# Performance work log

Measured on AMD Instinct MI355X. Metric: run time of the kernel, lower is better.

The kernel has to match this reference:

```python
import jax, jax.numpy as jnp
import numpy as np

B, S, H = 4, 1024, 2560          # batch, seq, hidden_size
E, K, F = 32, 6, 1536            # num_experts, top_k, moe_intermediate_size
SHARED_F = 2 * 1536              # moe_num_shared_experts * moe_intermediate_size
NORM_MIN = 1e-12                 # config.moe_norm_min


def setup_inputs() -> dict:
    key = jax.random.key(0)
    ks = jax.random.split(key, 9)
    rnd = lambda k, shape, scale=0.02: jax.random.normal(k, shape, dtype=jnp.float32) * scale
    return {
        "hidden_states": jax.random.normal(ks[0], (B, S, H), dtype=jnp.float32),
        "router_w": rnd(ks[1], (E, H)),              # Ernie4_5_MoeTopKRouter.weight (fp32)
        "router_bias": jnp.zeros((E,), jnp.float32),  # moe_statics.e_score_correction_bias
        "gate_w": rnd(ks[2], (E, H, F)),
        "up_w": rnd(ks[3], (E, H, F)),
        "down_w": rnd(ks[4], (E, F, H)),
        "shared_gate_w": rnd(ks[5], (H, SHARED_F)),
        "shared_up_w": rnd(ks[6], (H, SHARED_F)),
        "shared_down_w": rnd(ks[7], (SHARED_F, H)),
    }


def _mlp(x, gw, uw, dw):
    # Ernie4_5_MoeMLP: down( silu(gate(x)) * up(x) ), no biases
    return (jax.nn.silu(x @ gw) * (x @ uw)) @ dw


def _forward(hidden_states, router_w, router_bias, gate_w, up_w, down_w,
             shared_gate_w, shared_up_w, shared_down_w):
    T = B * S
    xt = hidden_states.reshape(T, H)

    # shared experts path (always-on dense MLP)
    shared_out = _mlp(xt, shared_gate_w, shared_up_w, shared_down_w)

    # router: fp32 linear -> softmax -> (+ correction bias) -> top-k -> renorm
    logits = xt.astype(jnp.float32) @ router_w.T            # [T, E]
    probs = jax.nn.softmax(logits, axis=-1)
    top_w, top_i = jax.lax.top_k(probs + router_bias[None, :], K)  # [T, K]
    top_w = top_w / jnp.clip(jnp.sum(top_w, axis=-1, keepdims=True), NORM_MIN)
    top_w = top_w.astype(hidden_states.dtype)

    # expert combine: loop over the fixed expert set; per-token combine weight
    # cw[t] = sum_k top_w[t,k] * (top_i[t,k] == e)  (matches one-hot dispatch +
    # index_add_ scatter combine of the original)
    out = jnp.zeros_like(xt)
    for e in range(E):
        cw = jnp.sum(jnp.where(top_i == e, top_w, 0.0), axis=-1)  # [T]
        y = _mlp(xt, gate_w[e], up_w[e], down_w[e])               # [T, H]
        out = out + cw[:, None] * y

    out = out + shared_out
    return out.reshape(B, S, H)


def reference(hidden_states, router_w, router_bias, gate_w, up_w, down_w,
              shared_gate_w, shared_up_w, shared_down_w):
    return _forward(hidden_states, router_w, router_bias, gate_w, up_w, down_w,
                    shared_gate_w, shared_up_w, shared_down_w)
```

## Files before the change

kernel.cpp:

```cpp
#include <hip/hip_runtime.h>
#include <hip/hip_bf16.h>
#include <math.h>

#define T_TOK 4096
#define HID   2560
#define NEXP  32
#define KTOP  6
#define FF    1536
#define SFF   3072
#define MAXP  (T_TOK*KTOP)

typedef __attribute__((ext_vector_type(8))) short short8;
typedef __attribute__((ext_vector_type(4))) float f32x4;

static __device__ __forceinline__ unsigned short f2bf(float x){
  return __builtin_bit_cast(unsigned short, (__bf16)x);
}

static __device__ __forceinline__ void gload_lds16(const void* g, void* l){
  __builtin_amdgcn_global_load_lds(
      (const __attribute__((address_space(1))) unsigned int*)g,
      (__attribute__((address_space(3))) unsigned int*)l, 16, 0, 0);
}

__global__ void k_cast_x(const float* __restrict__ x, unsigned short* __restrict__ xb){
  int i = (blockIdx.x * 256 + threadIdx.x) * 4;
  float4 v = *(const float4*)(x + i);
  ushort4 o;
  o.x = f2bf(v.x); o.y = f2bf(v.y); o.z = f2bf(v.z); o.w = f2bf(v.w);
  *(ushort4*)(xb + i) = o;
}

__global__ __launch_bounds__(256)
void k_transpose(const float* __restrict__ in, unsigned short* __restrict__ out,
                 const int R, const int C){
  const size_t bo = (size_t)blockIdx.z * (size_t)R * C;
  __shared__ unsigned short t2[64][72];
  const int r0 = blockIdx.y * 64, c0 = blockIdx.x * 64;
  const int tid = threadIdx.x;
  const int cr = tid & 15;
  const int rr = tid >> 4;
#pragma unroll
  for (int i = 0; i < 4; ++i){
    const int r = rr + 16*i;
    float4 v = *(const float4*)(in + bo + (size_t)(r0 + r)*C + c0 + cr*4);
    ushort4 p;
    p.x = f2bf(v.x); p.y = f2bf(v.y); p.z = f2bf(v.z); p.w = f2bf(v.w);
    *(ushort4*)(&t2[r][cr*4]) = p;
  }
  __syncthreads();
  const int rw = tid & 7;
  const int ro = tid >> 3;
#pragma unroll
  for (int i = 0; i < 2; ++i){
    const int c = ro + 32*i;
    ushort4 a, b;
    a.x = t2[rw*8+0][c]; a.y = t2[rw*8+1][c]; a.z = t2[rw*8+2][c]; a.w = t2[rw*8+3][c];
    b.x = t2[rw*8+4][c]; b.y = t2[rw*8+5][c]; b.z = t2[rw*8+6][c]; b.w = t2[rw*8+7][c];
    unsigned short* op = out + bo + (size_t)(c0 + c)*R + r0 + rw*8;
    *(ushort4*)(op)     = a;
    *(ushort4*)(op + 4) = b;
  }
}

__global__ void k_router(const float* __restrict__ x, const float* __restrict__ rw,
                         const float* __restrict__ rb, float* __restrict__ top_w,
                         int* __restrict__ top_i, int* __restrict__ counts){
  const int lane = threadIdx.x & 63;
  const int wv   = threadIdx.x >> 6;
  const int t    = blockIdx.x * 4 + wv;
  const float* xr = x + (size_t)t * HID;
  float xv[40];
#pragma unroll
  for (int i = 0; i < 40; ++i) xv[i] = xr[lane + 64*i];
  float sc[32];
  for (int e = 0; e < 32; ++e){
    const float* w = rw + (size_t)e * HID;
    float s = 0.f;
#pragma unroll
    for (int i = 0; i < 40; ++i) s = fmaf(xv[i], w[lane + 64*i], s);
#pragma unroll
    for (int o = 32; o; o >>= 1) s += __shfl_xor(s, o);
    sc[e] = s;
  }
  float mx = sc[0];
#pragma unroll
  for (int e = 1; e < 32; ++e) mx = fmaxf(mx, sc[e]);
  float se = 0.f;
#pragma unroll
  for (int e = 0; e < 32; ++e){ sc[e] = expf(sc[e] - mx); se += sc[e]; }
  const float inv = 1.f / se;
#pragma unroll
  for (int e = 0; e < 32; ++e) sc[e] = sc[e] * inv + rb[e];

  unsigned chosen = 0; float swv[KTOP]; int sid[KTOP]; float wsum = 0.f;
#pragma unroll
  for (int k = 0; k < KTOP; ++k){
    float bv = -1e30f; int bi = 0;
#pragma unroll
    for (int e = 0; e < 32; ++e){
      bool ok = !((chosen >> e) & 1u);
      if (ok && sc[e] > bv){ bv = sc[e]; bi = e; }
    }
    chosen |= 1u << bi; swv[k] = bv; sid[k] = bi; wsum += bv;
  }
  const float dn = fmaxf(wsum, 1e-12f);
  if (lane < KTOP){
    top_w[t*KTOP + lane] = swv[lane] / dn;
    top_i[t*KTOP + lane] = sid[lane];
    atomicAdd(counts + sid[lane], 1);
  }
}

__global__ void k_scan(const int* __restrict__ counts, int* __restrict__ offsets){
  if (threadIdx.x == 0){
    int a = 0;
    for (int e = 0; e < NEXP; ++e){ offsets[e] = a; a += counts[e]; }
    offsets[NEXP] = a;
  }
}

__global__ void k_scatter(const int* __restrict__ top_i, const float* __restrict__ top_w,
                          const int* __restrict__ offsets, int* __restrict__ cursor,
                          int* __restrict__ pair_tok, float* __restrict__ pair_w){
  const int t = blockIdx.x * 256 + threadIdx.x;
  if (t >= T_TOK) return;
#pragma unroll
  for (int k = 0; k < KTOP; ++k){
    int e = top_i[t*KTOP + k];
    int pos = offsets[e] + atomicAdd(cursor + e, 1);
    pair_tok[pos] = t;
    pair_w[pos]   = top_w[t*KTOP + k];
  }
}

template<bool EXP>
__global__ __launch_bounds__(256, 2)
void k_gateup3(const unsigned short* __restrict__ A,
               const unsigned short* __restrict__ BgT,
               const unsigned short* __restrict__ BuT,
               unsigned short* __restrict__ outp,
               const int* __restrict__ pair_tok,
               const int* __restrict__ counts, const int* __restrict__ offsets,
               const int N)
{
  constexpr int K = HID;
  constexpr int NT = K / 32;
  const int total = gridDim.x;
  const int phys  = blockIdx.x;
  const int logical = (phys & 7) * (total >> 3) + (phys >> 3);
  const int mt   = logical & 31;
  const int rest = logical >> 5;
  const int ntiles = N >> 7;
  const int n0 = (rest % ntiles) << 7;

  int M, base; const unsigned short *Bg, *Bu;
  if (EXP){
    const int e = rest / ntiles;
    M = counts[e]; base = offsets[e];
    const size_t wo = (size_t)e * (size_t)N * K;
    Bg = BgT + wo; Bu = BuT + wo;
  } else { M = T_TOK; base = 0; Bg = BgT; Bu = BuT; }
  if (mt * 128 >= M) return;

  __shared__ unsigned short As[3][4096];
  __shared__ unsigned short Bgs[3][4096];
  __shared__ unsigned short Bus[3][4096];

  const int tid  = threadIdx.x;
  const int lane = tid & 63;
  const int w    = tid >> 6;
  const int wr = w >> 1, wc = w & 1;

  const int lrow  = lane >> 2;
  const int chunk = lane & 3;
  const unsigned short *aptr[2], *bgptr[2], *buptr[2];
  int sw[2];
#pragma unroll
  for (int i = 0; i < 2; ++i){
    const int r = w*32 + i*16 + lrow;
    sw[i] = (chunk ^ (r & 3)) * 8;
    int ar = min(mt*128 + r, M - 1);
    int arow = EXP ? pair_tok[base + ar] : ar;
    aptr[i]  = A  + (size_t)arow * K;
    bgptr[i] = Bg + (size_t)(n0 + r) * K;
    buptr[i] = Bu + (size_t)(n0 + r) * K;
  }

  const f32x4 zero = {0.f,0.f,0.f,0.f};
  f32x4 accg[4][4], accu[4][4];
#pragma unroll
  for (int m = 0; m < 4; ++m)
#pragma unroll
    for (int n = 0; n < 4; ++n){ accg[m][n] = zero; accu[m][n] = zero; }

  const int am  = wr*64 + (lane & 15);
  const int bn_ = wc*64 + (lane & 15);
  const int fg  = ((lane >> 4) ^ (lane & 3)) * 16;

#define GU_STAGE(cb, k0)                                                   \
  {                                                                        \
    char* asd = (char*)As[cb]  + w*2048;                                   \
    char* bgd = (char*)Bgs[cb] + w*2048;                                   \
    char* bud = (char*)Bus[cb] + w*2048;                                   \
    _Pragma("unroll")                                                      \
    for (int i = 0; i < 2; ++i){                                           \
      gload_lds16(aptr[i]  + (k0) + sw[i], asd + i*1024);                  \
      gload_lds16(bgptr[i] + (k0) + sw[i], bgd + i*1024);                  \
      gload_lds16(buptr[i] + (k0) + sw[i], bud + i*1024);                  \
    }                                                                      \
  }

  GU_STAGE(0, 0)
  GU_STAGE(1, 32)
  asm volatile("s_waitcnt vmcnt(6)" ::: "memory");
  __builtin_amdgcn_s_barrier();

  int c0 = 0, c1 = 1, c2 = 2;
  for (int t = 0; t < NT; ++t){
    if (t + 2 < NT) GU_STAGE(c2, (t + 2) * 32)
    short8 af[4], bgf[4], buf_[4];
#pragma unroll
    for (int m = 0; m < 4; ++m)
      af[m] = *(const short8*)((const char*)As + c0*8192 + (am + m*16)*64 + fg);
#pragma unroll
    for (int n = 0; n < 4; ++n){
      bgf[n]  = *(const short8*)((const char*)Bgs + c0*8192 + (bn_ + n*16)*64 + fg);
      buf_[n] = *(const short8*)((const char*)Bus + c0*8192 + (bn_ + n*16)*64 + fg);
    }
#pragma unroll
    for (int m = 0; m < 4; ++m)
#pragma unroll
      for (int n = 0; n < 4; ++n){
        accg[m][n] = __builtin_amdgcn_mfma_f32_16x16x32_bf16(af[m], bgf[n],  accg[m][n], 0, 0, 0);
        accu[m][n] = __builtin_amdgcn_mfma_f32_16x16x32_bf16(af[m], buf_[n], accu[m][n], 0, 0, 0);
      }
    if (t + 2 < NT) asm volatile("s_waitcnt vmcnt(6)" ::: "memory");
    else            asm volatile("s_waitcnt vmcnt(0)" ::: "memory");
    __builtin_amdgcn_s_barrier();
    int tmp = c0; c0 = c1; c1 = c2; c2 = tmp;
  }
#undef GU_STAGE

#pragma unroll
  for (int m = 0; m < 4; ++m)
#pragma unroll
    for (int j = 0; j < 4; ++j){
      const int rr = mt*128 + wr*64 + m*16 + (lane >> 4)*4 + j;
      if (rr < M){
        unsigned short* orow = outp + (size_t)(base + rr) * N + n0 + wc*64 + (lane & 15);
#pragma unroll
        for (int n = 0; n < 4; ++n){
          float g = accg[m][n][j], u = accu[m][n][j];
          float s = (g / (1.f + expf(-g))) * u;
          orow[n*16] = f2bf(s);
        }
      }
    }
}

template<bool EXP>
__global__ __launch_bounds__(256, 3)
void k_down3(const unsigned short* __restrict__ Aact, const int K,
             const unsigned short* __restrict__ BT, float* __restrict__ outp,
             const int* __restrict__ pair_tok, const float* __restrict__ pair_w,
             const int* __restrict__ counts, const int* __restrict__ offsets)
{
  constexpr int N = HID;
  constexpr int ntiles = N >> 7;
  const int total = gridDim.x;
  const int phys  = blockIdx.x;
  const int logical = (phys & 7) * (total >> 3) + (phys >> 3);
  const int mt   = logical & 31;
  const int rest = logical >> 5;
  const int n0 = (rest % ntiles) << 7;

  int M, base; const unsigned short* Bw;
  if (EXP){
    const int e = rest / ntiles;
    M = counts[e]; base = offsets[e];
    Bw = BT + (size_t)e * (size_t)N * K;
  } else { M = T_TOK; base = 0; Bw = BT; }
  if (mt * 128 >= M) return;

  __shared__ unsigned short As[3][4096];
  __shared__ unsigned short Bs[3][4096];

  const int tid  = threadIdx.x;
  const int lane = tid & 63;
  const int w    = tid >> 6;
  const int wr = w >> 1, wc = w & 1;

  const int lrow  = lane >> 2;
  const int chunk = lane & 3;
  const unsigned short *aptr[2], *bptr[2];
  int sw[2];
#pragma unroll
  for (int i = 0; i < 2; ++i){
    const int r = w*32 + i*16 + lrow;
    sw[i] = (chunk ^ (r & 3)) * 8;
    int ar = min(mt*128 + r, M - 1);
    aptr[i] = Aact + (size_t)(base + ar) * K;
    bptr[i] = Bw + (size_t)(n0 + r) * K;
  }

  const f32x4 zero = {0.f,0.f,0.f,0.f};
  f32x4 acc[4][4];
#pragma unroll
  for (int m = 0; m < 4; ++m)
#pragma unroll
    for (int n = 0; n < 4; ++n) acc[m][n] = zero;

  const int am  = wr*64 + (lane & 15);
  const int bn_ = wc*64 + (lane & 15);
  const int fg  = ((lane >> 4) ^ (lane & 3)) * 16;

#define DN_STAGE(cb, k0)                                                   \
  {                                                                        \
    char* asd = (char*)As[cb] + w*2048;                                    \
    char* bsd = (char*)Bs[cb] + w*2048;                                    \
    _Pragma("unroll")                                                      \
    for (int i = 0; i < 2; ++i){                                           \
      gload_lds16(aptr[i] + (k0) + sw[i], asd + i*1024);                   \
      gload_lds16(bptr[i] + (k0) + sw[i], bsd + i*1024);                   \
    }                                                                      \
  }

  const int NT = K / 32;
  DN_STAGE(0, 0)
  DN_STAGE(1, 32)
  asm volatile("s_waitcnt vmcnt(4)" ::: "memory");
  __builtin_amdgcn_s_barrier();

  int c0 = 0, c1 = 1, c2 = 2;
  for (int t = 0; t < NT; ++t){
    if (t + 2 < NT) DN_STAGE(c2, (t + 2) * 32)
    short8 af[4], bf_[4];
#pragma unroll
    for (int m = 0; m < 4; ++m)
      af[m] = *(const short8*)((const char*)As + c0*8192 + (am + m*16)*64 + fg);
#pragma unroll
    for (int n = 0; n < 4; ++n)
      bf_[n] = *(const short8*)((const char*)Bs + c0*8192 + (bn_ + n*16)*64 + fg);
#pragma unroll
    for (int m = 0; m < 4; ++m)
#pragma unroll
      for (int n = 0; n < 4; ++n)
        acc[m][n] = __builtin_amdgcn_mfma_f32_16x16x32_bf16(af[m], bf_[n], acc[m][n], 0, 0, 0);
    if (t + 2 < NT) asm volatile("s_waitcnt vmcnt(4)" ::: "memory");
    else            asm volatile("s_waitcnt vmcnt(0)" ::: "memory");
    __builtin_amdgcn_s_barrier();
    int tmp = c0; c0 = c1; c1 = c2; c2 = tmp;
  }
#undef DN_STAGE

#pragma unroll
  for (int m = 0; m < 4; ++m)
#pragma unroll
    for (int j = 0; j < 4; ++j){
      const int rr = mt*128 + wr*64 + m*16 + (lane >> 4)*4 + j;
      if (rr < M){
        if (EXP){
          const int p = base + rr;
          const int tok = pair_tok[p];
          const float pw = pair_w[p];
          float* orow = outp + (size_t)tok * HID + n0 + wc*64 + (lane & 15);
#pragma unroll
          for (int n = 0; n < 4; ++n) atomicAdd(orow + n*16, acc[m][n][j] * pw);
        } else {
          float* orow = outp + (size_t)rr * HID + n0 + wc*64 + (lane & 15);
#pragma unroll
          for (int n = 0; n < 4; ++n) orow[n*16] = acc[m][n][j];
        }
      }
    }
}

extern "C" void kernel_launch(void* const* d_in, const int* in_sizes, int n_in,
                              void* d_out, int out_size, void* d_ws, size_t ws_size,
                              hipStream_t stream)
{
  (void)in_sizes; (void)n_in; (void)out_size; (void)ws_size;
  const float* hid = (const float*)d_in[0];
  const float* rw  = (const float*)d_in[1];
  const float* rb  = (const float*)d_in[2];
  const float* gw  = (const float*)d_in[3];
  const float* uw  = (const float*)d_in[4];
  const float* dw  = (const float*)d_in[5];
  const float* sgw = (const float*)d_in[6];
  const float* suw = (const float*)d_in[7];
  const float* sdw = (const float*)d_in[8];
  float* out = (float*)d_out;

  char* ws = (char*)d_ws;
  size_t o = 0;
  unsigned short* xb   = (unsigned short*)(ws + o); o += (size_t)T_TOK*HID*2;
  unsigned short* act  = (unsigned short*)(ws + o); o += (size_t)MAXP*FF*2;
  unsigned short* sact = (unsigned short*)(ws + o); o += (size_t)T_TOK*SFF*2;
  unsigned short* Wbuf = (unsigned short*)(ws + o);
  unsigned short* gT  = Wbuf;
  unsigned short* uT  = Wbuf + (size_t)NEXP*FF*HID;
  unsigned short* sgT = Wbuf + (size_t)2*NEXP*FF*HID;
  unsigned short* suT = sgT + (size_t)SFF*HID;
  unsigned short* dT  = Wbuf;
  unsigned short* sdT = Wbuf + (size_t)NEXP*FF*HID;
  o += (size_t)2*NEXP*FF*HID*2 + (size_t)2*SFF*HID*2;
  float* top_w    = (float*)(ws + o); o += (size_t)T_TOK*KTOP*4;
  int*   top_i    = (int*)(ws + o);   o += (size_t)T_TOK*KTOP*4;
  float* pair_w   = (float*)(ws + o); o += (size_t)MAXP*4;
  int*   pair_tok = (int*)(ws + o);   o += (size_t)MAXP*4;
  int*   counts   = (int*)(ws + o);   o += NEXP*4;
  int*   offsets  = (int*)(ws + o);   o += (NEXP+1)*4;
  int*   cursor   = (int*)(ws + o);   o += NEXP*4;

  hipMemsetAsync(counts, 0, (NEXP + (NEXP+1) + NEXP) * sizeof(int), stream);

  k_cast_x<<<(T_TOK*HID)/1024, 256, 0, stream>>>(hid, xb);
  k_router<<<T_TOK/4, 256, 0, stream>>>(hid, rw, rb, top_w, top_i, counts);
  k_scan<<<1, 64, 0, stream>>>(counts, offsets);
  k_scatter<<<T_TOK/256, 256, 0, stream>>>(top_i, top_w, offsets, cursor, pair_tok, pair_w);

  k_transpose<<<dim3(FF/64,  HID/64, NEXP), 256, 0, stream>>>(gw,  gT,  HID, FF);
  k_transpose<<<dim3(FF/64,  HID/64, NEXP), 256, 0, stream>>>(uw,  uT,  HID, FF);
  k_transpose<<<dim3(SFF/64, HID/64, 1),    256, 0, stream>>>(sgw, sgT, HID, SFF);
  k_transpose<<<dim3(SFF/64, HID/64, 1),    256, 0, stream>>>(suw, suT, HID, SFF);

  k_gateup3<true><<<32*(FF/128)*NEXP, 256, 0, stream>>>(
      xb, gT, uT, act, pair_tok, counts, offsets, FF);
  k_gateup3<false><<<32*(SFF/128), 256, 0, stream>>>(
      xb, sgT, suT, sact, nullptr, nullptr, nullptr, SFF);

  k_transpose<<<dim3(HID/64, FF/64,  NEXP), 256, 0, stream>>>(dw,  dT,  FF,  HID);
  k_transpose<<<dim3(HID/64, SFF/64, 1),    256, 0, stream>>>(sdw, sdT, SFF, HID);

  k_down3<false><<<32*(HID/128), 256, 0, stream>>>(
      sact, SFF, sdT, out, nullptr, nullptr, nullptr, nullptr);
  k_down3<true><<<32*(HID/128)*NEXP, 256, 0, stream>>>(
      act, FF, dT, out, pair_tok, pair_w, counts, offsets);
}
```

Before: 1.953 ms.

## Enlarge GEMM M-tile to 256 rows with 512-thread blocks and deeper pipeline

Gate/up and down GEMM kernels move to 512-thread blocks covering 256 token rows per tile instead of 128, so each loaded weight tile is reused across twice as many rows and weight traffic is cut. The gate/up kernel also goes from a 3-stage to a 4-stage LDS prefetch pipeline. The LDS swizzle and staging layout are redone to suit 8 waves. The costs are more LDS per block and wasted work on partial tiles for experts with few tokens, since per-expert M is only about 768 on average.

New measurement: 2.004 ms. +2.6%, slower.

```diff
diff --git a/kernel.cpp b/kernel.cpp
--- a/kernel.cpp
+++ b/kernel.cpp
@@ -135,8 +135,8 @@
 }
 
 template<bool EXP>
-__global__ __launch_bounds__(256, 2)
-void k_gateup3(const unsigned short* __restrict__ A,
+__global__ __launch_bounds__(512, 2)
+void k_gateup4(const unsigned short* __restrict__ A,
                const unsigned short* __restrict__ BgT,
                const unsigned short* __restrict__ BuT,
                unsigned short* __restrict__ outp,
@@ -149,8 +149,8 @@
   const int total = gridDim.x;
   const int phys  = blockIdx.x;
   const int logical = (phys & 7) * (total >> 3) + (phys >> 3);
-  const int mt   = logical & 31;
-  const int rest = logical >> 5;
+  const int mt   = logical & 15;
+  const int rest = logical >> 4;
   const int ntiles = N >> 7;
   const int n0 = (rest % ntiles) << 7;
 
@@ -161,11 +161,11 @@
     const size_t wo = (size_t)e * (size_t)N * K;
     Bg = BgT + wo; Bu = BuT + wo;
   } else { M = T_TOK; base = 0; Bg = BgT; Bu = BuT; }
-  if (mt * 128 >= M) return;
-
-  __shared__ unsigned short As[3][4096];
-  __shared__ unsigned short Bgs[3][4096];
-  __shared__ unsigned short Bus[3][4096];
+  if (mt * 256 >= M) return;
+
+  __shared__ unsigned short As[4][8192];
+  __shared__ unsigned short Bgs[4][4096];
+  __shared__ unsigned short Bus[4][4096];
 
   const int tid  = threadIdx.x;
   const int lane = tid & 63;
@@ -174,18 +174,23 @@
 
   const int lrow  = lane >> 2;
   const int chunk = lane & 3;
-  const unsigned short *aptr[2], *bgptr[2], *buptr[2];
-  int sw[2];
-#pragma unroll
-  for (int i = 0; i < 2; ++i){
-    const int r = w*32 + i*16 + lrow;
-    sw[i] = (chunk ^ (r & 3)) * 8;
-    int ar = min(mt*128 + r, M - 1);
-    int arow = EXP ? pair_tok[base + ar] : ar;
-    aptr[i]  = A  + (size_t)arow * K;
-    bgptr[i] = Bg + (size_t)(n0 + r) * K;
-    buptr[i] = Bu + (size_t)(n0 + r) * K;
-  }
+  const unsigned short *aptr0, *aptr1, *bgp, *bup;
+  {
+    const int r0 = w*16 + lrow;
+    const int r1 = 128 + r0;
+    const int k0a = (chunk ^ ((r0 >> 1) & 3)) * 8;
+    int ar0 = min(mt*256 + r0, M - 1);
+    int ar1 = min(mt*256 + r1, M - 1);
+    int row0 = EXP ? pair_tok[base + ar0] : ar0;
+    int row1 = EXP ? pair_tok[base + ar1] : ar1;
+    aptr0 = A + (size_t)row0 * K + k0a;
+    aptr1 = A + (size_t)row1 * K + k0a;
+    const int rb = w*16 + lrow;
+    const int k0b = (chunk ^ ((rb >> 1) & 3)) * 8;
+    bgp = Bg + (size_t)(n0 + rb) * K + k0b;
+    bup = Bu + (size_t)(n0 + rb) * K + k0b;
+  }
+  const int wdst = (w*16) * 64;
 
   const f32x4 zero = {0.f,0.f,0.f,0.f};
   f32x4 accg[4][4], accu[4][4];
@@ -196,33 +201,29 @@
 
   const int am  = wr*64 + (lane & 15);
   const int bn_ = wc*64 + (lane & 15);
-  const int fg  = ((lane >> 4) ^ (lane & 3)) * 16;
-
-#define GU_STAGE(cb, k0)                                                   \
-  {                                                                        \
-    char* asd = (char*)As[cb]  + w*2048;                                   \
-    char* bgd = (char*)Bgs[cb] + w*2048;                                   \
-    char* bud = (char*)Bus[cb] + w*2048;                                   \
-    _Pragma("unroll")                                                      \
-    for (int i = 0; i < 2; ++i){                                           \
-      gload_lds16(aptr[i]  + (k0) + sw[i], asd + i*1024);                  \
-      gload_lds16(bgptr[i] + (k0) + sw[i], bgd + i*1024);                  \
-      gload_lds16(buptr[i] + (k0) + sw[i], bud + i*1024);                  \
-    }                                                                      \
+  const int fg  = ((lane >> 4) ^ ((lane >> 1) & 3)) * 16;
+
+#define GU_STAGE(cb, k0)                                                    \
+  {                                                                         \
+    gload_lds16(aptr0 + (k0), (char*)As  + (cb)*16384 + wdst);              \
+    gload_lds16(aptr1 + (k0), (char*)As  + (cb)*16384 + 8192 + wdst);       \
+    gload_lds16(bgp   + (k0), (char*)Bgs + (cb)*8192 + wdst);               \
+    gload_lds16(bup   + (k0), (char*)Bus + (cb)*8192 + wdst);               \
   }
 
   GU_STAGE(0, 0)
   GU_STAGE(1, 32)
-  asm volatile("s_waitcnt vmcnt(6)" ::: "memory");
+  GU_STAGE(2, 64)
+  asm volatile("s_waitcnt vmcnt(8)" ::: "memory");
   __builtin_amdgcn_s_barrier();
 
-  int c0 = 0, c1 = 1, c2 = 2;
+  int c0 = 0, c1 = 1, c2 = 2, c3 = 3;
   for (int t = 0; t < NT; ++t){
-    if (t + 2 < NT) GU_STAGE(c2, (t + 2) * 32)
+    if (t + 3 < NT) GU_STAGE(c3, (t + 3) * 32)
     short8 af[4], bgf[4], buf_[4];
 #pragma unroll
     for (int m = 0; m < 4; ++m)
-      af[m] = *(const short8*)((const char*)As + c0*8192 + (am + m*16)*64 + fg);
+      af[m] = *(const short8*)((const char*)As + c0*16384 + (am + m*16)*64 + fg);
 #pragma unroll
     for (int n = 0; n < 4; ++n){
       bgf[n]  = *(const short8*)((const char*)Bgs + c0*8192 + (bn_ + n*16)*64 + fg);
@@ -235,10 +236,11 @@
         accg[m][n] = __builtin_amdgcn_mfma_f32_16x16x32_bf16(af[m], bgf[n],  accg[m][n], 0, 0, 0);
         accu[m][n] = __builtin_amdgcn_mfma_f32_16x16x32_bf16(af[m], buf_[n], accu[m][n], 0, 0, 0);
       }
-    if (t + 2 < NT) asm volatile("s_waitcnt vmcnt(6)" ::: "memory");
-    else            asm volatile("s_waitcnt vmcnt(0)" ::: "memory");
+    if (t + 3 < NT)      asm volatile("s_waitcnt vmcnt(8)" ::: "memory");
+    else if (t + 2 < NT) asm volatile("s_waitcnt vmcnt(4)" ::: "memory");
+    else                 asm volatile("s_waitcnt vmcnt(0)" ::: "memory");
     __builtin_amdgcn_s_barrier();
-    int tmp = c0; c0 = c1; c1 = c2; c2 = tmp;
+    int tmp = c0; c0 = c1; c1 = c2; c2 = c3; c3 = tmp;
   }
 #undef GU_STAGE
 
@@ -246,7 +248,7 @@
   for (int m = 0; m < 4; ++m)
 #pragma unroll
     for (int j = 0; j < 4; ++j){
-      const int rr = mt*128 + wr*64 + m*16 + (lane >> 4)*4 + j;
+      const int rr = mt*256 + wr*64 + m*16 + (lane >> 4)*4 + j;
       if (rr < M){
         unsigned short* orow = outp + (size_t)(base + rr) * N + n0 + wc*64 + (lane & 15);
 #pragma unroll
@@ -260,8 +262,8 @@
 }
 
 template<bool EXP>
-__global__ __launch_bounds__(256, 3)
-void k_down3(const unsigned short* __restrict__ Aact, const int K,
+__global__ __launch_bounds__(512, 4)
+void k_down4(const unsigned short* __restrict__ Aact, const int K,
              const unsigned short* __restrict__ BT, float* __restrict__ outp,
              const int* __restrict__ pair_tok, const float* __restrict__ pair_w,
              const int* __restrict__ counts, const int* __restrict__ offsets)
@@ -271,8 +273,8 @@
   const int total = gridDim.x;
   const int phys  = blockIdx.x;
   const int logical = (phys & 7) * (total >> 3) + (phys >> 3);
-  const int mt   = logical & 31;
-  const int rest = logical >> 5;
+  const int mt   = logical & 15;
+  const int rest = logical >> 4;
   const int n0 = (rest % ntiles) << 7;
 
   int M, base; const unsigned short* Bw;
@@ -281,9 +283,9 @@
     M = counts[e]; base = offsets[e];
     Bw = BT + (size_t)e * (size_t)N * K;
   } else { M = T_TOK; base = 0; Bw = BT; }
-  if (mt * 128 >= M) return;
-
-  __shared__ unsigned short As[3][4096];
+  if (mt * 256 >= M) return;
+
+  __shared__ unsigned short As[3][8192];
   __shared__ unsigned short Bs[3][4096];
 
   const int tid  = threadIdx.x;
@@ -293,16 +295,20 @@
 
   const int lrow  = lane >> 2;
   const int chunk = lane & 3;
-  const unsigned short *aptr[2], *bptr[2];
-  int sw[2];
-#pragma unroll
-  for (int i = 0; i < 2; ++i){
-    const int r = w*32 + i*16 + lrow;
-    sw[i] = (chunk ^ (r & 3)) * 8;
-    int ar = min(mt*128 + r, M - 1);
-    aptr[i] = Aact + (size_t)(base + ar) * K;
-    bptr[i] = Bw + (size_t)(n0 + r) * K;
-  }
+  const unsigned short *aptr0, *aptr1, *bp;
+  {
+    const int r0 = w*16 + lrow;
+    const int r1 = 128 + r0;
+    const int k0a = (chunk ^ ((r0 >> 1) & 3)) * 8;
+    int ar0 = min(mt*256 + r0, M - 1);
+    int ar1 = min(mt*256 + r1, M - 1);
+    aptr0 = Aact + (size_t)(base + ar0) * K + k0a;
+    aptr1 = Aact + (size_t)(base + ar1) * K + k0a;
+    const int rb = w*16 + lrow;
+    const int k0b = (chunk ^ ((rb >> 1) & 3)) * 8;
+    bp = Bw + (size_t)(n0 + rb) * K + k0b;
+  }
+  const int wdst = (w*16) * 64;
 
   const f32x4 zero = {0.f,0.f,0.f,0.f};
   f32x4 acc[4][4];
@@ -313,23 +319,19 @@
 
   const int am  = wr*64 + (lane & 15);
   const int bn_ = wc*64 + (lane & 15);
-  const int fg  = ((lane >> 4) ^ (lane & 3)) * 16;
-
-#define DN_STAGE(cb, k0)                                                   \
-  {                                                                        \
-    char* asd = (char*)As[cb] + w*2048;                                    \
-    char* bsd = (char*)Bs[cb] + w*2048;                                    \
-    _Pragma("unroll")                                                      \
-    for (int i = 0; i < 2; ++i){                                           \
-      gload_lds16(aptr[i] + (k0) + sw[i], asd + i*1024);                   \
-      gload_lds16(bptr[i] + (k0) + sw[i], bsd + i*1024);                   \
-    }                                                                      \
+  const int fg  = ((lane >> 4) ^ ((lane >> 1) & 3)) * 16;
+
+#define DN_STAGE(cb, k0)                                                    \
+  {                                                                         \
+    gload_lds16(aptr0 + (k0), (char*)As + (cb)*16384 + wdst);               \
+    gload_lds16(aptr1 + (k0), (char*)As + (cb)*16384 + 8192 + wdst);        \
+    gload_lds16(bp    + (k0), (char*)Bs + (cb)*8192 + wdst);                \
   }
 
   const int NT = K / 32;
   DN_STAGE(0, 0)
   DN_STAGE(1, 32)
-  asm volatile("s_waitcnt vmcnt(4)" ::: "memory");
+  asm volatile("s_waitcnt vmcnt(3)" ::: "memory");
   __builtin_amdgcn_s_barrier();
 
   int c0 = 0, c1 = 1, c2 = 2;
@@ -338,7 +340,7 @@
     short8 af[4], bf_[4];
 #pragma unroll
     for (int m = 0; m < 4; ++m)
-      af[m] = *(const short8*)((const char*)As + c0*8192 + (am + m*16)*64 + fg);
+      af[m] = *(const short8*)((const char*)As + c0*16384 + (am + m*16)*64 + fg);
 #pragma unroll
     for (int n = 0; n < 4; ++n)
       bf_[n] = *(const short8*)((const char*)Bs + c0*8192 + (bn_ + n*16)*64 + fg);
@@ -347,7 +349,7 @@
 #pragma unroll
       for (int n = 0; n < 4; ++n)
         acc[m][n] = __builtin_amdgcn_mfma_f32_16x16x32_bf16(af[m], bf_[n], acc[m][n], 0, 0, 0);
-    if (t + 2 < NT) asm volatile("s_waitcnt vmcnt(4)" ::: "memory");
+    if (t + 2 < NT) asm volatile("s_waitcnt vmcnt(3)" ::: "memory");
     else            asm volatile("s_waitcnt vmcnt(0)" ::: "memory");
     __builtin_amdgcn_s_barrier();
     int tmp = c0; c0 = c1; c1 = c2; c2 = tmp;
@@ -358,7 +360,7 @@
   for (int m = 0; m < 4; ++m)
 #pragma unroll
     for (int j = 0; j < 4; ++j){
-      const int rr = mt*128 + wr*64 + m*16 + (lane >> 4)*4 + j;
+      const int rr = mt*256 + wr*64 + m*16 + (lane >> 4)*4 + j;
       if (rr < M){
         if (EXP){
           const int p = base + rr;
@@ -425,16 +427,16 @@
   k_transpose<<<dim3(SFF/64, HID/64, 1),    256, 0, stream>>>(sgw, sgT, HID, SFF);
   k_transpose<<<dim3(SFF/64, HID/64, 1),    256, 0, stream>>>(suw, suT, HID, SFF);
 
-  k_gateup3<true><<<32*(FF/128)*NEXP, 256, 0, stream>>>(
+  k_gateup4<true><<<16*(FF/128)*NEXP, 512, 0, stream>>>(
       xb, gT, uT, act, pair_tok, counts, offsets, FF);
-  k_gateup3<false><<<32*(SFF/128), 256, 0, stream>>>(
+  k_gateup4<false><<<16*(SFF/128), 512, 0, stream>>>(
       xb, sgT, suT, sact, nullptr, nullptr, nullptr, SFF);
 
   k_transpose<<<dim3(HID/64, FF/64,  NEXP), 256, 0, stream>>>(dw,  dT,  FF,  HID);
   k_transpose<<<dim3(HID/64, SFF/64, 1),    256, 0, stream>>>(sdw, sdT, SFF, HID);
 
-  k_down3<false><<<32*(HID/128), 256, 0, stream>>>(
+  k_down4<false><<<16*(HID/128), 512, 0, stream>>>(
       sact, SFF, sdT, out, nullptr, nullptr, nullptr, nullptr);
-  k_down3<true><<<32*(HID/128)*NEXP, 256, 0, stream>>>(
+  k_down4<true><<<16*(HID/128)*NEXP, 512, 0, stream>>>(
       act, FF, dT, out, pair_tok, pair_w, counts, offsets);
 }
```
